# Optimization experiments

Hardware: AMD Instinct MI355X
Metric: run time of the kernel (lower is better)

Reference implementation:

```python
import jax, jax.numpy as jnp
import numpy as np

N = 8192


def setup_inputs() -> dict:
    key = jax.random.key(0)
    k1, k2, k3, k4, k5, k6 = jax.random.split(key, 6)
    return {
        "thresholds": jax.random.uniform(k1, (N,), dtype=jnp.float32),
        "rules_left": jax.random.randint(k2, (N,), 0, 36, dtype=jnp.int32),
        "rules_right": jax.random.randint(k3, (N,), 0, 36, dtype=jnp.int32),
        "binary_ops": jax.random.randint(k4, (N,), 0, 4, dtype=jnp.int32),
        "left": jax.random.randint(k5, (N,), 0, N, dtype=jnp.int32),
        "right": jax.random.randint(k6, (N,), 0, N, dtype=jnp.int32),
    }


def reference(thresholds, rules_left, rules_right, binary_ops, left, right):
    """DAGGenome.get_active_mask: propagate reachability from node 0 along
    left/right child edges via an N-step scan (faithful to the original)."""
    n = thresholds.shape[0]
    left_valid = (left >= 0) & (left < n)
    right_valid = (right >= 0) & (right < n)
    safe_left = jnp.where(left_valid, left, 0)
    safe_right = jnp.where(right_valid, right, 0)

    def step(reachable, _):
        # scatter: children of currently reachable nodes become reachable
        l = jnp.zeros(n, jnp.bool_).at[safe_left].set(reachable & left_valid)
        r = jnp.zeros(n, jnp.bool_).at[safe_right].set(reachable & right_valid)
        return reachable | l | r, None

    init = jnp.zeros(n, jnp.bool_).at[0].set(True)
    mask, _ = jax.lax.scan(step, init, None, length=n)
    return mask
```

## Files before the change

### kernel.cpp

```cpp
#include <hip/hip_runtime.h>


#define NN   8192
#define NT   512
#define PER  (NN / NT)
#define SENT NN
#define MAXE 512

__global__ __launch_bounds__(NT) void dag_reach_kernel(
    const int* __restrict__ left,
    const int* __restrict__ right,
    int* __restrict__ out)
{
    __shared__ int           lpI[NN + 1];
    __shared__ int           rpI[NN + 1];
    __shared__ unsigned char reach[NN + 4];
    __shared__ int           flags[MAXE];

    const int tid = threadIdx.x;

    int lv[PER], rv[PER];
    #pragma unroll
    for (int k = 0; k < PER; ++k) {
        const int i = tid + k * NT;
        lv[k] = left[i];
        rv[k] = right[i];
    }

    #pragma unroll
    for (int k = 0; k < PER; ++k) {
        const int i = tid + k * NT;
        lpI[i] = -1;
        rpI[i] = -1;
    }
    int* reach32 = (int*)reach;
    #pragma unroll
    for (int k = 0; k < (NN / 4) / NT; ++k)
        reach32[tid + k * NT] = 0;
    if (tid == 0) {
        reach32[NN / 4] = 0;
        lpI[SENT] = -1;
        rpI[SENT] = -1;
        reach[0] = 1;
    }
    flags[tid] = 0;
    __syncthreads();

    #pragma unroll
    for (int k = 0; k < PER; ++k) {
        const int i = tid + k * NT;
        const int l = lv[k];
        const int r = rv[k];
        if ((unsigned)l < (unsigned)NN) atomicMax(&lpI[l], i);
        if ((unsigned)r < (unsigned)NN) atomicMax(&rpI[r], i);
    }
    __syncthreads();

    int lp[PER], rp[PER];
    unsigned pend = 0, rmask = 0;
    #pragma unroll
    for (int k = 0; k < PER; ++k) {
        const int i = tid + k * NT;
        const int a = lpI[i];
        const int b = rpI[i];
        lp[k] = (a < 0) ? SENT : a;
        rp[k] = (b < 0) ? SENT : b;
        if ((a >= 0 || b >= 0) && i != 0) pend |= (1u << k);
    }
    if (tid == 0) rmask |= 1u;

    for (int e = 0; ; ++e) {
        int fprev = 1;
        if (e > 0) fprev = flags[e - 1];

        if (pend) {
            int prog = 0;
            #pragma unroll
            for (int k = 0; k < PER; ++k) {
                if (pend & (1u << k)) {
                    if (reach[lp[k]] | reach[rp[k]]) {
                        reach[tid + k * NT] = 1;
                        rmask |= (1u << k);
                        pend  &= ~(1u << k);
                        prog = 1;
                    }
                }
            }
            if (prog) flags[e] = 1;
        }

        if (fprev == 0) break;
        if (e >= MAXE - 2) break;
        __syncthreads();
    }

    #pragma unroll
    for (int k = 0; k < PER; ++k) {
        out[tid + k * NT] = (int)((rmask >> k) & 1u);
    }
}

extern "C" void kernel_launch(void* const* d_in, const int* in_sizes, int n_in,
                              void* d_out, int out_size, void* d_ws, size_t ws_size,
                              hipStream_t stream) {
    const int* left  = (const int*)d_in[4];
    const int* right = (const int*)d_in[5];
    int* out = (int*)d_out;

    dag_reach_kernel<<<1, NT, 0, stream>>>(left, right, out);
}
```

Before: 12.88 us.

## Halve threads, alternate sweep direction, and exit right after a no-progress barrier

Switches to 256 threads with 32 nodes each and alternates forward and backward sweeps across each thread's nodes, so reachability can travel further within one iteration. Termination now checks the current iteration's progress flag just after the barrier instead of the previous one, removing one extra iteration. The intent is fewer barrier rounds and cheaper barriers, at the cost of more serial work per thread and a lower cap on iterations.

```diff
diff --git a/kernel.cpp b/kernel.cpp
--- a/kernel.cpp
+++ b/kernel.cpp
@@ -2,20 +2,20 @@
 
 
 #define NN   8192
-#define NT   512
+#define NT   256
 #define PER  (NN / NT)
 #define SENT NN
-#define MAXE 512
+#define MAXE 256
 
 __global__ __launch_bounds__(NT) void dag_reach_kernel(
     const int* __restrict__ left,
     const int* __restrict__ right,
     int* __restrict__ out)
 {
-    __shared__ int           lpI[NN + 1];
-    __shared__ int           rpI[NN + 1];
-    __shared__ unsigned char reach[NN + 4];
-    __shared__ int           flags[MAXE];
+    __shared__ int lpI[NN + 1];
+    __shared__ int rpI[NN + 1];
+    __shared__ __align__(16) unsigned char reach[NN + 16];
+    __shared__ int flags[MAXE];
 
     const int tid = threadIdx.x;
 
@@ -33,12 +33,10 @@
         lpI[i] = -1;
         rpI[i] = -1;
     }
-    int* reach32 = (int*)reach;
-    #pragma unroll
-    for (int k = 0; k < (NN / 4) / NT; ++k)
-        reach32[tid + k * NT] = 0;
+    ((int4*)reach)[tid]      = make_int4(0, 0, 0, 0);
+    ((int4*)reach)[tid + NT] = make_int4(0, 0, 0, 0);
     if (tid == 0) {
-        reach32[NN / 4] = 0;
+        *(int4*)(reach + NN) = make_int4(0, 0, 0, 0);
         lpI[SENT] = -1;
         rpI[SENT] = -1;
         reach[0] = 1;
@@ -69,29 +67,37 @@
     }
     if (tid == 0) rmask |= 1u;
 
+    #pragma unroll 1
     for (int e = 0; ; ++e) {
-        int fprev = 1;
-        if (e > 0) fprev = flags[e - 1];
-
         if (pend) {
             int prog = 0;
-            #pragma unroll
-            for (int k = 0; k < PER; ++k) {
-                if (pend & (1u << k)) {
-                    if (reach[lp[k]] | reach[rp[k]]) {
-                        reach[tid + k * NT] = 1;
-                        rmask |= (1u << k);
-                        pend  &= ~(1u << k);
-                        prog = 1;
+            if ((e & 1) == 0) {
+                #pragma unroll
+                for (int k = 0; k < PER; ++k) {
+                    const unsigned b = 1u << k;
+                    if (pend & b) {
+                        if (reach[lp[k]] | reach[rp[k]]) {
+                            reach[tid + k * NT] = 1;
+                            rmask |= b; pend &= ~b; prog = 1;
+                        }
+                    }
+                }
+            } else {
+                #pragma unroll
+                for (int k = PER - 1; k >= 0; --k) {
+                    const unsigned b = 1u << k;
+                    if (pend & b) {
+                        if (reach[lp[k]] | reach[rp[k]]) {
+                            reach[tid + k * NT] = 1;
+                            rmask |= b; pend &= ~b; prog = 1;
+                        }
                     }
                 }
             }
             if (prog) flags[e] = 1;
         }
-
-        if (fprev == 0) break;
-        if (e >= MAXE - 2) break;
         __syncthreads();
+        if (e >= MAXE - 2 || flags[e] == 0) break;
     }
 
     #pragma unroll
```

Measured after the change: 14.96 us. 1.16x slower.
